# Kernel optimization log

Measured on AMD Instinct MI355X. Metric: run time of the kernel, lower is better.

Reference implementation:

```python
import jax, jax.numpy as jnp
import numpy as np

N_TX, N_USER = 100000, 50000
F_TX, F_USER = 128, 64
HID, H, OUT = 64, 4, 32
E = 500000
SLOPE = 0.2  # PyG GATConv default negative_slope


def _gat(x_src, x_dst, src, dst, W, a_src, a_dst, bias, heads, ch, concat, n_dst):
    # PyG GATConv (shared lin for src/dst, add_self_loops=False)
    hs = (x_src @ W).reshape(-1, heads, ch)          # [Ns,H,C]
    hd = (x_dst @ W).reshape(-1, heads, ch)          # [Nd,H,C]
    als = jnp.einsum('nhc,hc->nh', hs, a_src)        # alpha_src per node
    ald = jnp.einsum('nhc,hc->nh', hd, a_dst)
    e = jax.nn.leaky_relu(als[src] + ald[dst], SLOPE)        # [E,H]
    emax = jax.ops.segment_max(e, dst, num_segments=n_dst)   # softmax per dst
    ex = jnp.exp(e - emax[dst])
    den = jax.ops.segment_sum(ex, dst, num_segments=n_dst)
    alpha = ex / (den[dst] + 1e-16)
    out = jax.ops.segment_sum(hs[src] * alpha[:, :, None], dst, num_segments=n_dst)
    out = out.reshape(n_dst, heads * ch) if concat else out.mean(axis=1)
    return out + bias


def setup_inputs() -> dict:
    key = jax.random.key(0)
    ks = iter(jax.random.split(key, 40))
    def nrm(shape, s=0.05):
        return jax.random.normal(next(ks), shape, dtype=jnp.float32) * s
    inp = {}
    inp['x_tx'] = jax.random.normal(next(ks), (N_TX, F_TX), dtype=jnp.float32)
    inp['x_user'] = jax.random.normal(next(ks), (N_USER, F_USER), dtype=jnp.float32)
    src_u = jax.random.randint(next(ks), (E,), 0, N_USER)
    dst_t = jax.random.randint(next(ks), (E,), 0, N_TX)
    inp['ei_u2t'] = jnp.stack([src_u, dst_t]).astype(jnp.int32)
    src_t = jax.random.randint(next(ks), (E,), 0, N_TX)
    dst_u = jax.random.randint(next(ks), (E,), 0, N_USER)
    inp['ei_t2u'] = jnp.stack([src_t, dst_u]).astype(jnp.int32)
    inp['Wp_tx'] = nrm((F_TX, HID)); inp['bp_tx'] = jnp.zeros((HID,), jnp.float32)
    inp['Wp_user'] = nrm((F_USER, HID)); inp['bp_user'] = jnp.zeros((HID,), jnp.float32)
    for et in ('u2t', 't2u'):
        inp[f'W1_{et}'] = nrm((HID, H * HID))
        inp[f'as1_{et}'] = nrm((H, HID)); inp[f'ad1_{et}'] = nrm((H, HID))
        inp[f'b1_{et}'] = jnp.zeros((H * HID,), jnp.float32)
        inp[f'W2_{et}'] = nrm((H * HID, OUT))
        inp[f'as2_{et}'] = nrm((1, OUT)); inp[f'ad2_{et}'] = nrm((1, OUT))
        inp[f'b2_{et}'] = jnp.zeros((OUT,), jnp.float32)
    inp['Wc'] = nrm((OUT, 1)); inp['bc'] = jnp.zeros((1,), jnp.float32)
    return inp


def reference(x_tx, x_user, ei_u2t, ei_t2u, Wp_tx, bp_tx, Wp_user, bp_user,
              W1_u2t, as1_u2t, ad1_u2t, b1_u2t, W1_t2u, as1_t2u, ad1_t2u, b1_t2u,
              W2_u2t, as2_u2t, ad2_u2t, b2_u2t, W2_t2u, as2_t2u, ad2_t2u, b2_t2u,
              Wc, bc):
    elu = jax.nn.elu
    h_tx = elu(x_tx @ Wp_tx + bp_tx)
    h_us = elu(x_user @ Wp_user + bp_user)
    # conv1: heads=H, concat=True (HeteroConv sum -> each dst has one edge type)
    t1 = _gat(h_us, h_tx, ei_u2t[0], ei_u2t[1], W1_u2t, as1_u2t, ad1_u2t, b1_u2t, H, HID, True, N_TX)
    u1 = _gat(h_tx, h_us, ei_t2u[0], ei_t2u[1], W1_t2u, as1_t2u, ad1_t2u, b1_t2u, H, HID, True, N_USER)
    t1, u1 = elu(t1), elu(u1)
    # conv2: heads=1, concat=False; only 'transaction' output feeds classifier
    t2 = elu(_gat(u1, t1, ei_u2t[0], ei_u2t[1], W2_u2t, as2_u2t, ad2_u2t, b2_u2t, 1, OUT, False, N_TX))
    return (t2 @ Wc + bc)[:, 0]
```

## Files before the change

### kernel.cpp

```cpp
#include <hip/hip_runtime.h>
#include <hip/hip_bf16.h>
#include <math.h>

#define N_TX   100000
#define N_USER 50000
#define F_TX   128
#define F_USER 64
#define HID    64
#define NH     4
#define OUTC   32
#define NE     500000
#define HC1    256
#define SLOPE  0.2f
#define NB_T   391
#define NB_U   196

__device__ __forceinline__ float elu_f(float x) { return x > 0.f ? x : (expf(x) - 1.f); }
__device__ __forceinline__ float lrelu_exp_fast(float x) { x = x > 0.f ? x : SLOPE * x; return __expf(x); }

#define ACC_STEP(i, XS, WV) \
    acc[i][0] = fmaf((XS), (WV).x, acc[i][0]); \
    acc[i][1] = fmaf((XS), (WV).y, acc[i][1]); \
    acc[i][2] = fmaf((XS), (WV).z, acc[i][2]); \
    acc[i][3] = fmaf((XS), (WV).w, acc[i][3]);
#define ACC4(i, XV) \
    ACC_STEP(i, (XV).x, w0) ACC_STEP(i, (XV).y, w1) \
    ACC_STEP(i, (XV).z, w2) ACC_STEP(i, (XV).w, w3)

__global__ __launch_bounds__(256) void gemm_kernel(const float* __restrict__ A,
    const float* __restrict__ B, const float* __restrict__ bias,
    float* __restrict__ C, int N, int K, int M, int act)
{
    __shared__ float As[16][68];
    __shared__ float Bs[16][68];
    const int tid = threadIdx.x;
    const int tx = tid % 16, ty = tid / 16;
    const int row0 = blockIdx.y * 64, col0 = blockIdx.x * 64;
    float acc[4][4] = {};
    for (int k0 = 0; k0 < K; k0 += 16) {
        #pragma unroll
        for (int i = 0; i < 4; ++i) {
            int idx = tid * 4 + i;
            int r = idx >> 4, kk = idx & 15;
            int gr = row0 + r;
            As[kk][r] = (gr < N) ? A[(size_t)gr * K + (k0 + kk)] : 0.f;
        }
        #pragma unroll
        for (int i = 0; i < 4; ++i) {
            int idx = tid * 4 + i;
            int kk = idx >> 6, c = idx & 63;
            int gc = col0 + c;
            Bs[kk][c] = (gc < M) ? B[(size_t)(k0 + kk) * M + gc] : 0.f;
        }
        __syncthreads();
        #pragma unroll 2
        for (int kk = 0; kk < 16; ++kk) {
            const float4 av = *(const float4*)(&As[kk][ty * 4]);
            const float4 bv = *(const float4*)(&Bs[kk][tx * 4]);
            ACC_STEP(0, av.x, bv)
            ACC_STEP(1, av.y, bv)
            ACC_STEP(2, av.z, bv)
            ACC_STEP(3, av.w, bv)
        }
        __syncthreads();
    }
    #pragma unroll
    for (int i = 0; i < 4; ++i) {
        int r = row0 + ty * 4 + i;
        if (r >= N) continue;
        #pragma unroll
        for (int j = 0; j < 4; ++j) {
            int c = col0 + tx * 4 + j;
            if (c >= M) continue;
            float v = acc[i][j] + (bias ? bias[c] : 0.f);
            if (act == 1) v = elu_f(v);
            C[(size_t)r * M + c] = v;
        }
    }
}

__global__ __launch_bounds__(256) void gemm_proj_attn_dual(
    const float* __restrict__ A1, const float* __restrict__ B1, const float* __restrict__ bias1,
    float* __restrict__ C1, int N1, int K1,
    const float* __restrict__ Ma1, float* __restrict__ oa1,
    const float* __restrict__ Mb1, float* __restrict__ ob1, int NB1,
    const float* __restrict__ A2, const float* __restrict__ B2, const float* __restrict__ bias2,
    float* __restrict__ C2, int N2, int K2,
    const float* __restrict__ Ma2, float* __restrict__ oa2,
    const float* __restrict__ Mb2, float* __restrict__ ob2)
{
    __shared__ float As[16][68];
    __shared__ float Bs[16][68];
    const int tid = threadIdx.x;
    const int tx = tid % 16, ty = tid / 16;
    const float* A; const float* B; const float* bias; float* C; int N, K;
    const float* Ma; float* oa; const float* Mb; float* ob; int row0;
    if ((int)blockIdx.y < NB1) {
        A = A1; B = B1; bias = bias1; C = C1; N = N1; K = K1;
        Ma = Ma1; oa = oa1; Mb = Mb1; ob = ob1;
        row0 = blockIdx.y * 64;
    } else {
        A = A2; B = B2; bias = bias2; C = C2; N = N2; K = K2;
        Ma = Ma2; oa = oa2; Mb = Mb2; ob = ob2;
        row0 = (blockIdx.y - NB1) * 64;
    }
    float acc[4][4] = {};
    for (int k0 = 0; k0 < K; k0 += 16) {
        #pragma unroll
        for (int i = 0; i < 4; ++i) {
            int idx = tid * 4 + i;
            int r = idx >> 4, kk = idx & 15;
            int gr = row0 + r;
            As[kk][r] = (gr < N) ? A[(size_t)gr * K + (k0 + kk)] : 0.f;
        }
        #pragma unroll
        for (int i = 0; i < 4; ++i) {
            int idx = tid * 4 + i;
            int kk = idx >> 6, c = idx & 63;
            Bs[kk][c] = B[(size_t)(k0 + kk) * 64 + c];
        }
        __syncthreads();
        #pragma unroll 2
        for (int kk = 0; kk < 16; ++kk) {
            const float4 av = *(const float4*)(&As[kk][ty * 4]);
            const float4 bv = *(const float4*)(&Bs[kk][tx * 4]);
            ACC_STEP(0, av.x, bv)
            ACC_STEP(1, av.y, bv)
            ACC_STEP(2, av.z, bv)
            ACC_STEP(3, av.w, bv)
        }
        __syncthreads();
    }
    const float4 ma0 = *(const float4*)(Ma + (tx * 4 + 0) * 4);
    const float4 ma1 = *(const float4*)(Ma + (tx * 4 + 1) * 4);
    const float4 ma2 = *(const float4*)(Ma + (tx * 4 + 2) * 4);
    const float4 ma3 = *(const float4*)(Ma + (tx * 4 + 3) * 4);
    const float4 mb0 = *(const float4*)(Mb + (tx * 4 + 0) * 4);
    const float4 mb1 = *(const float4*)(Mb + (tx * 4 + 1) * 4);
    const float4 mb2 = *(const float4*)(Mb + (tx * 4 + 2) * 4);
    const float4 mb3 = *(const float4*)(Mb + (tx * 4 + 3) * 4);
    const float4 bb  = *(const float4*)(bias + tx * 4);
    #pragma unroll
    for (int i = 0; i < 4; ++i) {
        int r = row0 + ty * 4 + i;
        bool wr = (r < N);
        float v0 = acc[i][0] + bb.x; v0 = v0 > 0.f ? v0 : (expf(v0) - 1.f);
        float v1 = acc[i][1] + bb.y; v1 = v1 > 0.f ? v1 : (expf(v1) - 1.f);
        float v2 = acc[i][2] + bb.z; v2 = v2 > 0.f ? v2 : (expf(v2) - 1.f);
        float v3 = acc[i][3] + bb.w; v3 = v3 > 0.f ? v3 : (expf(v3) - 1.f);
        if (wr) *(float4*)(C + (size_t)r * 64 + tx * 4) = make_float4(v0, v1, v2, v3);
        float pax = v0 * ma0.x + v1 * ma1.x + v2 * ma2.x + v3 * ma3.x;
        float pay = v0 * ma0.y + v1 * ma1.y + v2 * ma2.y + v3 * ma3.y;
        float paz = v0 * ma0.z + v1 * ma1.z + v2 * ma2.z + v3 * ma3.z;
        float paw = v0 * ma0.w + v1 * ma1.w + v2 * ma2.w + v3 * ma3.w;
        float pbx = v0 * mb0.x + v1 * mb1.x + v2 * mb2.x + v3 * mb3.x;
        float pby = v0 * mb0.y + v1 * mb1.y + v2 * mb2.y + v3 * mb3.y;
        float pbz = v0 * mb0.z + v1 * mb1.z + v2 * mb2.z + v3 * mb3.z;
        float pbw = v0 * mb0.w + v1 * mb1.w + v2 * mb2.w + v3 * mb3.w;
        #pragma unroll
        for (int off = 1; off < 16; off <<= 1) {
            pax += __shfl_xor(pax, off); pay += __shfl_xor(pay, off);
            paz += __shfl_xor(paz, off); paw += __shfl_xor(paw, off);
            pbx += __shfl_xor(pbx, off); pby += __shfl_xor(pby, off);
            pbz += __shfl_xor(pbz, off); pbw += __shfl_xor(pbw, off);
        }
        if (tx == 0 && wr) {
            *(float4*)(oa + (size_t)r * 4) = make_float4(pax, pay, paz, paw);
            *(float4*)(ob + (size_t)r * 4) = make_float4(pbx, pby, pbz, pbw);
        }
    }
}

struct AVArgs  { const float* W; const float* a; float* out; int K; int H; int C; };
struct AVArgs6 { AVArgs t[6]; };

__global__ void attn_vecs_kernel(AVArgs6 args)
{
    AVArgs A = args.t[blockIdx.x];
    int tid = threadIdx.x;
    if (tid < A.K * A.H) {
        int k = tid % A.K, h = tid / A.K;
        float s = 0.f;
        const float* wrow = A.W + (size_t)k * (A.H * A.C) + h * A.C;
        const float* arow = A.a + h * A.C;
        for (int c = 0; c < A.C; ++c) s += wrow[c] * arow[c];
        A.out[k * A.H + h] = s;
    }
}

__global__ __launch_bounds__(256) void hist2_kernel(const int* __restrict__ dst_t,
    const int* __restrict__ dst_u, int* __restrict__ deg_t, int* __restrict__ deg_u)
{
    int e = blockIdx.x * 256 + threadIdx.x;
    if (e < NE) atomicAdd(&deg_t[dst_t[e]], 1);
    else {
        e -= NE;
        if (e < NE) atomicAdd(&deg_u[dst_u[e]], 1);
    }
}

__global__ __launch_bounds__(256) void block_sum2_kernel(const int* __restrict__ deg_t,
    int* __restrict__ bsum_t, const int* __restrict__ deg_u, int* __restrict__ bsum_u)
{
    __shared__ int lds[256];
    int b = blockIdx.x, t = threadIdx.x;
    const int* deg; int* bsum; int Nd, lb;
    if (b < NB_T) { deg = deg_t; bsum = bsum_t; Nd = N_TX; lb = b; }
    else         { deg = deg_u; bsum = bsum_u; Nd = N_USER; lb = b - NB_T; }
    int i = lb * 256 + t;
    lds[t] = (i < Nd) ? deg[i] : 0;
    __syncthreads();
    for (int o = 128; o > 0; o >>= 1) {
        if (t < o) lds[t] += lds[t + o];
        __syncthreads();
    }
    if (t == 0) bsum[lb] = lds[0];
}

__global__ __launch_bounds__(512) void scan_bsum2_kernel(int* __restrict__ bt,
    int* __restrict__ bu)
{
    __shared__ int lds[512];
    int t = threadIdx.x;
    {
        int v = (t < NB_T) ? bt[t] : 0;
        lds[t] = v;
        __syncthreads();
        for (int o = 1; o < 512; o <<= 1) {
            int x = (t >= o) ? lds[t - o] : 0;
            __syncthreads();
            lds[t] += x;
            __syncthreads();
        }
        if (t < NB_T) bt[t] = lds[t] - v;
        __syncthreads();
    }
    {
        int v = (t < NB_U) ? bu[t] : 0;
        lds[t] = v;
        __syncthreads();
        for (int o = 1; o < 512; o <<= 1) {
            int x = (t >= o) ? lds[t - o] : 0;
            __syncthreads();
            lds[t] += x;
            __syncthreads();
        }
        if (t < NB_U) bu[t] = lds[t] - v;
    }
}

__global__ __launch_bounds__(256) void scan_final2_kernel(
    const int* __restrict__ deg_t, const int* __restrict__ be_t,
    int* __restrict__ rowptr_t, int* __restrict__ cur_t,
    const int* __restrict__ deg_u, const int* __restrict__ be_u,
    int* __restrict__ rowptr_u, int* __restrict__ cur_u)
{
    __shared__ int lds[256];
    int b = blockIdx.x, t = threadIdx.x;
    const int* deg; const int* be; int* rowptr; int* cursor; int Nd, lb;
    if (b < NB_T) { deg = deg_t; be = be_t; rowptr = rowptr_t; cursor = cur_t; Nd = N_TX; lb = b; }
    else         { deg = deg_u; be = be_u; rowptr = rowptr_u; cursor = cur_u; Nd = N_USER; lb = b - NB_T; }
    int i = lb * 256 + t;
    int v = (i < Nd) ? deg[i] : 0;
    lds[t] = v;
    __syncthreads();
    for (int o = 1; o < 256; o <<= 1) {
        int x = (t >= o) ? lds[t - o] : 0;
        __syncthreads();
        lds[t] += x;
        __syncthreads();
    }
    int excl = lds[t] - v + be[lb];
    if (i < Nd) {
        rowptr[i] = excl;
        cursor[i] = excl;
        if (i == Nd - 1) rowptr[Nd] = NE;
    }
}

__global__ __launch_bounds__(256) void scatter_ew_kernel(
    const int* __restrict__ src, const int* __restrict__ dst,
    int* __restrict__ cur, float* __restrict__ rec,
    const float* __restrict__ als, const float* __restrict__ ald)
{
    int e = blockIdx.x * 256 + threadIdx.x;
    if (e >= NE) return;
    int s = src[e], d = dst[e];
    int p = atomicAdd(&cur[d], 1);
    float4 a = *(const float4*)(als + (size_t)s * 4);
    float4 b = *(const float4*)(ald + (size_t)d * 4);
    float4 w;
    w.x = lrelu_exp_fast(a.x + b.x);
    w.y = lrelu_exp_fast(a.y + b.y);
    w.z = lrelu_exp_fast(a.z + b.z);
    w.w = lrelu_exp_fast(a.w + b.w);
    float* r8 = rec + (size_t)p * 8;
    *(float4*)(r8)     = w;
    *(float4*)(r8 + 4) = make_float4(__int_as_float(s), 0.f, 0.f, 0.f);
}

__device__ __forceinline__ void acc_edge(int i, int lane,
    const float* __restrict__ rec, const float* __restrict__ hsrc,
    float& a0, float& a1, float& a2, float& a3,
    float& w0, float& w1, float& w2, float& w3)
{
    const float* r8 = rec + (size_t)i * 8;
    float4 e = *(const float4*)(r8);
    int s = __float_as_int(r8[4]);
    float x = hsrc[(size_t)s * 64 + lane];
    a0 = fmaf(e.x, x, a0); w0 += e.x;
    a1 = fmaf(e.y, x, a1); w1 += e.y;
    a2 = fmaf(e.z, x, a2); w2 += e.z;
    a3 = fmaf(e.w, x, a3); w3 += e.w;
}

__global__ __launch_bounds__(256) void agg_conv1_kernel(const int* __restrict__ rowptr,
    const float* __restrict__ rec, const float* __restrict__ hsrc,
    float* __restrict__ agg, int Nd)
{
    int d = blockIdx.x * 4 + (threadIdx.x >> 6);
    int lane = threadIdx.x & 63;
    if (d >= Nd) return;
    int beg = rowptr[d], end = rowptr[d + 1];
    float a0 = 0.f, a1 = 0.f, a2 = 0.f, a3 = 0.f;
    float w0 = 0.f, w1 = 0.f, w2 = 0.f, w3 = 0.f;
    int i = beg;
    for (; i + 2 <= end; i += 2) {
        acc_edge(i,     lane, rec, hsrc, a0, a1, a2, a3, w0, w1, w2, w3);
        acc_edge(i + 1, lane, rec, hsrc, a0, a1, a2, a3, w0, w1, w2, w3);
    }
    if (i < end)
        acc_edge(i, lane, rec, hsrc, a0, a1, a2, a3, w0, w1, w2, w3);
    float* o = agg + (size_t)d * 256;
    o[lane]       = a0 / (w0 + 1e-16f);
    o[64 + lane]  = a1 / (w1 + 1e-16f);
    o[128 + lane] = a2 / (w2 + 1e-16f);
    o[192 + lane] = a3 / (w3 + 1e-16f);
}

__global__ __launch_bounds__(256) void transform_v6(
    const float* __restrict__ agg, const float* __restrict__ W1,
    const float* __restrict__ b1, const float* __restrict__ vvec,
    float* __restrict__ dot_part, float* __restrict__ rows_out,
    int Nd, int writeRows)
{
    constexpr int SXP = 68;
    __shared__ float sX[64 * SXP];
    __shared__ float sW[64 * 64];
    const int tid  = threadIdx.x;
    const int w    = tid >> 6;
    const int lane = tid & 63;
    const int h    = blockIdx.y;
    const int base = blockIdx.x * 64;

    #pragma unroll
    for (int it = 0; it < 4; ++it) {
        int r  = w * 16 + it * 4 + (lane >> 4);
        int c0 = (lane & 15) * 4;
        int g  = base + r;
        float4 v = make_float4(0.f, 0.f, 0.f, 0.f);
        if (g < Nd) v = *(const float4*)(agg + (size_t)g * 256 + h * 64 + c0);
        *(float4*)(sX + r * SXP + c0) = v;
    }
    #pragma unroll
    for (int it = 0; it < 4; ++it) {
        int c    = w * 16 + it * 4 + (lane >> 4);
        int col0 = (lane & 15) * 4;
        *(float4*)(sW + c * 64 + col0) =
            *(const float4*)(W1 + (size_t)c * 256 + h * 64 + col0);
    }
    __syncthreads();

    const int tx = tid & 15;
    const int ty = tid >> 4;
    float acc[4][4] = {};

    #pragma unroll 1
    for (int c0 = 0; c0 < 64; c0 += 4) {
        const float4 x0 = *(const float4*)(sX + (ty * 4 + 0) * SXP + c0);
        const float4 x1 = *(const float4*)(sX + (ty * 4 + 1) * SXP + c0);
        const float4 x2 = *(const float4*)(sX + (ty * 4 + 2) * SXP + c0);
        const float4 x3 = *(const float4*)(sX + (ty * 4 + 3) * SXP + c0);
        const float4 w0 = *(const float4*)(sW + (c0 + 0) * 64 + tx * 4);
        const float4 w1 = *(const float4*)(sW + (c0 + 1) * 64 + tx * 4);
        const float4 w2 = *(const float4*)(sW + (c0 + 2) * 64 + tx * 4);
        const float4 w3 = *(const float4*)(sW + (c0 + 3) * 64 + tx * 4);
        ACC4(0, x0)
        ACC4(1, x1)
        ACC4(2, x2)
        ACC4(3, x3)
    }

    const float4 bb = *(const float4*)(b1   + h * 64 + tx * 4);
    const float4 vv = *(const float4*)(vvec + h * 64 + tx * 4);
    float* dp = dot_part + (size_t)h * Nd;
    #pragma unroll
    for (int i = 0; i < 4; ++i) {
        int g = base + ty * 4 + i;
        if (g >= Nd) continue;
        float v0 = acc[i][0] + bb.x; v0 = v0 > 0.f ? v0 : (expf(v0) - 1.f);
        float v1 = acc[i][1] + bb.y; v1 = v1 > 0.f ? v1 : (expf(v1) - 1.f);
        float v2 = acc[i][2] + bb.z; v2 = v2 > 0.f ? v2 : (expf(v2) - 1.f);
        float v3 = acc[i][3] + bb.w; v3 = v3 > 0.f ? v3 : (expf(v3) - 1.f);
        if (writeRows)
            *(float4*)(rows_out + (size_t)g * 256 + h * 64 + tx * 4) =
                make_float4(v0, v1, v2, v3);
        float s = v0 * vv.x + v1 * vv.y + v2 * vv.z + v3 * vv.w;
        s += __shfl_xor(s, 1); s += __shfl_xor(s, 2);
        s += __shfl_xor(s, 4); s += __shfl_xor(s, 8);
        if (tx == 0) dp[g] = s;
    }
}

__global__ __launch_bounds__(256) void combine_parts(
    const float* __restrict__ ap, float* __restrict__ o1, int N1,
    const float* __restrict__ bp, float* __restrict__ o2, int N2)
{
    int i = blockIdx.x * 256 + threadIdx.x;
    if (i < N1) {
        o1[i] = ap[i] + ap[N1 + i] + ap[2 * N1 + i] + ap[3 * N1 + i];
    } else {
        int j = i - N1;
        if (j < N2)
            o2[j] = bp[j] + bp[N2 + j] + bp[2 * N2 + j] + bp[3 * N2 + j];
    }
}

__global__ __launch_bounds__(256) void conv2_fused_kernel(const int* __restrict__ rowptr,
    const float* __restrict__ rec, const float* __restrict__ hs2,
    const float* __restrict__ als2, const float* __restrict__ ald2,
    const float* __restrict__ b2, const float* __restrict__ Wc, const float* __restrict__ bc,
    float* __restrict__ out, int Nd)
{
    int d = blockIdx.x * 4 + (threadIdx.x >> 6);
    int lane = threadIdx.x & 63;
    if (d >= Nd) return;
    int beg = rowptr[d], end = rowptr[d + 1];
    float aldd = ald2[d];
    int half = lane >> 5, c = lane & 31;
    float acc = 0.f, wsum = 0.f;
    for (int i = beg + half; i < end; i += 2) {
        int s = __float_as_int(rec[(size_t)i * 8 + 4]);
        float w = lrelu_exp_fast(als2[s] + aldd);
        acc = fmaf(w, hs2[(size_t)s * 32 + c], acc);
        wsum += w;
    }
    acc  += __shfl_down(acc, 32);
    wsum += __shfl_down(wsum, 32);
    float val = 0.f;
    if (lane < 32) {
        float t2 = acc / (wsum + 1e-16f) + b2[c];
        t2 = t2 > 0.f ? t2 : (expf(t2) - 1.f);
        val = t2 * Wc[c];
    }
    #pragma unroll
    for (int o = 16; o > 0; o >>= 1) val += __shfl_down(val, o);
    if (lane == 0) out[d] = val + bc[0];
}

extern "C" void kernel_launch(void* const* d_in, const int* in_sizes, int n_in,
                              void* d_out, int out_size, void* d_ws, size_t ws_size,
                              hipStream_t stream)
{
    const float* x_tx    = (const float*)d_in[0];
    const float* x_user  = (const float*)d_in[1];
    const int*   ei_u2t  = (const int*)d_in[2];
    const int*   ei_t2u  = (const int*)d_in[3];
    const float* Wp_tx   = (const float*)d_in[4];
    const float* bp_tx   = (const float*)d_in[5];
    const float* Wp_user = (const float*)d_in[6];
    const float* bp_user = (const float*)d_in[7];
    const float* W1_u2t  = (const float*)d_in[8];
    const float* as1_u2t = (const float*)d_in[9];
    const float* ad1_u2t = (const float*)d_in[10];
    const float* b1_u2t  = (const float*)d_in[11];
    const float* W2_u2t  = (const float*)d_in[12];
    const float* as2_u2t = (const float*)d_in[13];
    const float* ad2_u2t = (const float*)d_in[14];
    const float* b2_u2t  = (const float*)d_in[15];
    const float* W1_t2u  = (const float*)d_in[16];
    const float* as1_t2u = (const float*)d_in[17];
    const float* ad1_t2u = (const float*)d_in[18];
    const float* b1_t2u  = (const float*)d_in[19];
    const float* Wc      = (const float*)d_in[24];
    const float* bc      = (const float*)d_in[25];
    float* out = (float*)d_out;
    float* ws  = (float*)d_ws;

    const int* src_u2t = ei_u2t;
    const int* dst_u2t = ei_u2t + NE;
    const int* src_t2u = ei_t2u;
    const int* dst_u   = ei_t2u + NE;

    float* h_tx   = ws;
    float* h_us   = ws + 6400000;
    float* hs2    = ws + 9600000;
    float* als2   = ws + 11200000;
    float* ald2   = ws + 11250000;
    float* als_us = ws + 11350000;
    float* ald_us = ws + 11550000;
    float* als_tx = ws + 11750000;
    float* ald_tx = ws + 12150000;
    float* agg    = ws + 12550000;
    float* avec   = ws + 38150000;
    float* ald2p = hs2;
    float* als2p = hs2 + 400000;
    float* rec_t  = ws + 38152000;
    float* rec_u  = agg + 12800000;
    int* ibase    = (int*)(ws + 42152000);
    int* deg_t    = ibase;
    int* deg_u    = ibase + 100000;
    int* rowptr_t = ibase + 150000;
    int* cur_t    = ibase + 250001;
    int* rowptr_u = ibase + 350001;
    int* cur_u    = ibase + 400002;
    int* bsum_t   = ibase + 450052;
    int* bsum_u   = ibase + 450564;

    float* Msrc_u2t = avec + 0;
    float* Mdst_u2t = avec + 256;
    float* Msrc_t2u = avec + 512;
    float* Mdst_t2u = avec + 768;
    float* vsrc2    = avec + 1024;
    float* vdst2    = avec + 1280;

    AVArgs6 av;
    av.t[0] = { W1_u2t, as1_u2t, Msrc_u2t, HID, NH, HID };
    av.t[1] = { W1_u2t, ad1_u2t, Mdst_u2t, HID, NH, HID };
    av.t[2] = { W1_t2u, as1_t2u, Msrc_t2u, HID, NH, HID };
    av.t[3] = { W1_t2u, ad1_t2u, Mdst_t2u, HID, NH, HID };
    av.t[4] = { W2_u2t, as2_u2t, vsrc2, HC1, 1, OUTC };
    av.t[5] = { W2_u2t, ad2_u2t, vdst2, HC1, 1, OUTC };
    attn_vecs_kernel<<<6, 256, 0, stream>>>(av);

    hipMemsetAsync(deg_t, 0, 150000 * sizeof(int), stream);

    hist2_kernel<<<(2 * NE + 255) / 256, 256, 0, stream>>>(dst_u2t, dst_u, deg_t, deg_u);
    block_sum2_kernel<<<NB_T + NB_U, 256, 0, stream>>>(deg_t, bsum_t, deg_u, bsum_u);
    scan_bsum2_kernel<<<1, 512, 0, stream>>>(bsum_t, bsum_u);
    scan_final2_kernel<<<NB_T + NB_U, 256, 0, stream>>>(
        deg_t, bsum_t, rowptr_t, cur_t, deg_u, bsum_u, rowptr_u, cur_u);

    const int NB1 = (N_TX + 63) / 64;
    const int NB2 = (N_USER + 63) / 64;
    gemm_proj_attn_dual<<<dim3(1, NB1 + NB2), 256, 0, stream>>>(
        x_tx, Wp_tx, bp_tx, h_tx, N_TX, F_TX,
        Mdst_u2t, ald_tx, Msrc_t2u, als_tx, NB1,
        x_user, Wp_user, bp_user, h_us, N_USER, F_USER,
        Msrc_u2t, als_us, Mdst_t2u, ald_us);

    scatter_ew_kernel<<<(NE + 255) / 256, 256, 0, stream>>>(
        src_u2t, dst_u2t, cur_t, rec_t, als_us, ald_tx);
    agg_conv1_kernel<<<(N_TX + 3) / 4, 256, 0, stream>>>(
        rowptr_t, rec_t, h_us, agg, N_TX);
    transform_v6<<<dim3((N_TX + 63) / 64, NH), 256, 0, stream>>>(
        agg, W1_u2t, b1_u2t, vdst2, ald2p, nullptr, N_TX, 0);

    scatter_ew_kernel<<<(NE + 255) / 256, 256, 0, stream>>>(
        src_t2u, dst_u, cur_u, rec_u, als_tx, ald_us);
    agg_conv1_kernel<<<(N_USER + 3) / 4, 256, 0, stream>>>(
        rowptr_u, rec_u, h_tx, agg, N_USER);
    transform_v6<<<dim3((N_USER + 63) / 64, NH), 256, 0, stream>>>(
        agg, W1_t2u, b1_t2u, vsrc2, als2p, agg, N_USER, 1);
    float* u1 = agg;

    combine_parts<<<(N_TX + N_USER + 255) / 256, 256, 0, stream>>>(
        ald2p, ald2, N_TX, als2p, als2, N_USER);

    gemm_kernel<<<dim3(1, (N_USER + 63) / 64), 256, 0, stream>>>(
        u1, W2_u2t, nullptr, hs2, N_USER, HC1, OUTC, 0);
    conv2_fused_kernel<<<(N_TX + 3) / 4, 256, 0, stream>>>(
        rowptr_t, rec_t, hs2, als2, ald2, b2_u2t, Wc, bc, out, N_TX);
}
```

Baseline: 564.2 us.

## Fuse conv2 linear projection into per-head conv1 transform with partial sums

The user-side conv1 transform no longer writes the full 256-wide u1 rows to global memory. Each head block instead keeps its ELU output in shared memory and multiplies it by its 64-row slice of W2, writing per-head partial hs2 values. A combined reduction kernel then sums the four partials, alongside the existing attention-dot partial sums. This removes the u1 write and re-read and the separate GEMM launch, at the cost of writing and re-reading four 32-wide partial buffers.

```diff
diff --git a/kernel.cpp b/kernel.cpp
--- a/kernel.cpp
+++ b/kernel.cpp
@@ -26,58 +26,6 @@
 #define ACC4(i, XV) \
     ACC_STEP(i, (XV).x, w0) ACC_STEP(i, (XV).y, w1) \
     ACC_STEP(i, (XV).z, w2) ACC_STEP(i, (XV).w, w3)
-
-__global__ __launch_bounds__(256) void gemm_kernel(const float* __restrict__ A,
-    const float* __restrict__ B, const float* __restrict__ bias,
-    float* __restrict__ C, int N, int K, int M, int act)
-{
-    __shared__ float As[16][68];
-    __shared__ float Bs[16][68];
-    const int tid = threadIdx.x;
-    const int tx = tid % 16, ty = tid / 16;
-    const int row0 = blockIdx.y * 64, col0 = blockIdx.x * 64;
-    float acc[4][4] = {};
-    for (int k0 = 0; k0 < K; k0 += 16) {
-        #pragma unroll
-        for (int i = 0; i < 4; ++i) {
-            int idx = tid * 4 + i;
-            int r = idx >> 4, kk = idx & 15;
-            int gr = row0 + r;
-            As[kk][r] = (gr < N) ? A[(size_t)gr * K + (k0 + kk)] : 0.f;
-        }
-        #pragma unroll
-        for (int i = 0; i < 4; ++i) {
-            int idx = tid * 4 + i;
-            int kk = idx >> 6, c = idx & 63;
-            int gc = col0 + c;
-            Bs[kk][c] = (gc < M) ? B[(size_t)(k0 + kk) * M + gc] : 0.f;
-        }
-        __syncthreads();
-        #pragma unroll 2
-        for (int kk = 0; kk < 16; ++kk) {
-            const float4 av = *(const float4*)(&As[kk][ty * 4]);
-            const float4 bv = *(const float4*)(&Bs[kk][tx * 4]);
-            ACC_STEP(0, av.x, bv)
-            ACC_STEP(1, av.y, bv)
-            ACC_STEP(2, av.z, bv)
-            ACC_STEP(3, av.w, bv)
-        }
-        __syncthreads();
-    }
-    #pragma unroll
-    for (int i = 0; i < 4; ++i) {
-        int r = row0 + ty * 4 + i;
-        if (r >= N) continue;
-        #pragma unroll
-        for (int j = 0; j < 4; ++j) {
-            int c = col0 + tx * 4 + j;
-            if (c >= M) continue;
-            float v = acc[i][j] + (bias ? bias[c] : 0.f);
-            if (act == 1) v = elu_f(v);
-            C[(size_t)r * M + c] = v;
-        }
-    }
-}
 
 __global__ __launch_bounds__(256) void gemm_proj_attn_dual(
     const float* __restrict__ A1, const float* __restrict__ B1, const float* __restrict__ bias1,
@@ -338,11 +286,11 @@
     o[192 + lane] = a3 / (w3 + 1e-16f);
 }
 
-__global__ __launch_bounds__(256) void transform_v6(
+__global__ __launch_bounds__(256) void transform_v10(
     const float* __restrict__ agg, const float* __restrict__ W1,
     const float* __restrict__ b1, const float* __restrict__ vvec,
-    float* __restrict__ dot_part, float* __restrict__ rows_out,
-    int Nd, int writeRows)
+    float* __restrict__ dot_part, const float* __restrict__ W2,
+    float* __restrict__ hs2p, int Nd, int fuse2)
 {
     constexpr int SXP = 68;
     __shared__ float sX[64 * SXP];
@@ -390,6 +338,7 @@
         ACC4(2, x2)
         ACC4(3, x3)
     }
+    __syncthreads();
 
     const float4 bb = *(const float4*)(b1   + h * 64 + tx * 4);
     const float4 vv = *(const float4*)(vvec + h * 64 + tx * 4);
@@ -397,32 +346,73 @@
     #pragma unroll
     for (int i = 0; i < 4; ++i) {
         int g = base + ty * 4 + i;
-        if (g >= Nd) continue;
         float v0 = acc[i][0] + bb.x; v0 = v0 > 0.f ? v0 : (expf(v0) - 1.f);
         float v1 = acc[i][1] + bb.y; v1 = v1 > 0.f ? v1 : (expf(v1) - 1.f);
         float v2 = acc[i][2] + bb.z; v2 = v2 > 0.f ? v2 : (expf(v2) - 1.f);
         float v3 = acc[i][3] + bb.w; v3 = v3 > 0.f ? v3 : (expf(v3) - 1.f);
-        if (writeRows)
-            *(float4*)(rows_out + (size_t)g * 256 + h * 64 + tx * 4) =
-                make_float4(v0, v1, v2, v3);
+        if (fuse2)
+            *(float4*)(sX + (ty * 4 + i) * SXP + tx * 4) = make_float4(v0, v1, v2, v3);
         float s = v0 * vv.x + v1 * vv.y + v2 * vv.z + v3 * vv.w;
         s += __shfl_xor(s, 1); s += __shfl_xor(s, 2);
         s += __shfl_xor(s, 4); s += __shfl_xor(s, 8);
-        if (tx == 0) dp[g] = s;
-    }
-}
-
-__global__ __launch_bounds__(256) void combine_parts(
-    const float* __restrict__ ap, float* __restrict__ o1, int N1,
-    const float* __restrict__ bp, float* __restrict__ o2, int N2)
+        if (tx == 0 && g < Nd) dp[g] = s;
+    }
+
+    if (!fuse2) return;
+
+    {
+        int idx0 = tid * 8;
+        int r = idx0 >> 5, j0 = idx0 & 31;
+        const float* wsrc = W2 + (size_t)(h * 64 + r) * 32 + j0;
+        *(float4*)(sW + r * 32 + j0)     = *(const float4*)(wsrc);
+        *(float4*)(sW + r * 32 + j0 + 4) = *(const float4*)(wsrc + 4);
+    }
+    __syncthreads();
+
+    float a2[4][2] = {};
+    #pragma unroll 1
+    for (int r0 = 0; r0 < 64; r0 += 4) {
+        const float4 y0 = *(const float4*)(sX + (ty * 4 + 0) * SXP + r0);
+        const float4 y1 = *(const float4*)(sX + (ty * 4 + 1) * SXP + r0);
+        const float4 y2 = *(const float4*)(sX + (ty * 4 + 2) * SXP + r0);
+        const float4 y3 = *(const float4*)(sX + (ty * 4 + 3) * SXP + r0);
+        const float2 wA = *(const float2*)(sW + (r0 + 0) * 32 + tx * 2);
+        const float2 wB = *(const float2*)(sW + (r0 + 1) * 32 + tx * 2);
+        const float2 wC = *(const float2*)(sW + (r0 + 2) * 32 + tx * 2);
+        const float2 wD = *(const float2*)(sW + (r0 + 3) * 32 + tx * 2);
+        #define P2(i, YV) \
+            a2[i][0] = fmaf((YV).x, wA.x, a2[i][0]); a2[i][1] = fmaf((YV).x, wA.y, a2[i][1]); \
+            a2[i][0] = fmaf((YV).y, wB.x, a2[i][0]); a2[i][1] = fmaf((YV).y, wB.y, a2[i][1]); \
+            a2[i][0] = fmaf((YV).z, wC.x, a2[i][0]); a2[i][1] = fmaf((YV).z, wC.y, a2[i][1]); \
+            a2[i][0] = fmaf((YV).w, wD.x, a2[i][0]); a2[i][1] = fmaf((YV).w, wD.y, a2[i][1]);
+        P2(0, y0) P2(1, y1) P2(2, y2) P2(3, y3)
+        #undef P2
+    }
+    float* hp = hs2p + (size_t)h * ((size_t)N_USER * 32);
+    #pragma unroll
+    for (int i = 0; i < 4; ++i) {
+        int g = base + ty * 4 + i;
+        if (g < Nd)
+            *(float2*)(hp + (size_t)g * 32 + tx * 2) = make_float2(a2[i][0], a2[i][1]);
+    }
+}
+
+__global__ __launch_bounds__(256) void combine3_kernel(
+    const float* __restrict__ ap, float* __restrict__ o1,
+    const float* __restrict__ bp, float* __restrict__ o2,
+    const float* __restrict__ hp, float* __restrict__ o3)
 {
     int i = blockIdx.x * 256 + threadIdx.x;
-    if (i < N1) {
-        o1[i] = ap[i] + ap[N1 + i] + ap[2 * N1 + i] + ap[3 * N1 + i];
+    if (i < N_TX) {
+        o1[i] = ap[i] + ap[N_TX + i] + ap[2 * N_TX + i] + ap[3 * N_TX + i];
+    } else if (i < N_TX + N_USER) {
+        int j = i - N_TX;
+        o2[j] = bp[j] + bp[N_USER + j] + bp[2 * N_USER + j] + bp[3 * N_USER + j];
     } else {
-        int j = i - N1;
-        if (j < N2)
-            o2[j] = bp[j] + bp[N2 + j] + bp[2 * N2 + j] + bp[3 * N2 + j];
+        int k = i - N_TX - N_USER;
+        const int HS = N_USER * 32;
+        if (k < HS)
+            o3[k] = hp[k] + hp[HS + k] + hp[2 * HS + k] + hp[3 * HS + k];
     }
 }
 
@@ -494,7 +484,7 @@
 
     float* h_tx   = ws;
     float* h_us   = ws + 6400000;
-    float* hs2    = ws + 9600000;
+    float* parts  = ws + 9600000;
     float* als2   = ws + 11200000;
     float* ald2   = ws + 11250000;
     float* als_us = ws + 11350000;
@@ -503,10 +493,12 @@
     float* ald_tx = ws + 12150000;
     float* agg    = ws + 12550000;
     float* avec   = ws + 38150000;
-    float* ald2p = hs2;
-    float* als2p = hs2 + 400000;
+    float* ald2p = parts;
+    float* als2p = parts + 400000;
     float* rec_t  = ws + 38152000;
     float* rec_u  = agg + 12800000;
+    float* hs2p   = agg + 17000000;
+    float* hs2f   = agg + 23500000;
     int* ibase    = (int*)(ws + 42152000);
     int* deg_t    = ibase;
     int* deg_u    = ibase + 100000;
@@ -553,22 +545,19 @@
         src_u2t, dst_u2t, cur_t, rec_t, als_us, ald_tx);
     agg_conv1_kernel<<<(N_TX + 3) / 4, 256, 0, stream>>>(
         rowptr_t, rec_t, h_us, agg, N_TX);
-    transform_v6<<<dim3((N_TX + 63) / 64, NH), 256, 0, stream>>>(
-        agg, W1_u2t, b1_u2t, vdst2, ald2p, nullptr, N_TX, 0);
+    transform_v10<<<dim3((N_TX + 63) / 64, NH), 256, 0, stream>>>(
+        agg, W1_u2t, b1_u2t, vdst2, ald2p, nullptr, nullptr, N_TX, 0);
 
     scatter_ew_kernel<<<(NE + 255) / 256, 256, 0, stream>>>(
         src_t2u, dst_u, cur_u, rec_u, als_tx, ald_us);
     agg_conv1_kernel<<<(N_USER + 3) / 4, 256, 0, stream>>>(
         rowptr_u, rec_u, h_tx, agg, N_USER);
-    transform_v6<<<dim3((N_USER + 63) / 64, NH), 256, 0, stream>>>(
-        agg, W1_t2u, b1_t2u, vsrc2, als2p, agg, N_USER, 1);
-    float* u1 = agg;
-
-    combine_parts<<<(N_TX + N_USER + 255) / 256, 256, 0, stream>>>(
-        ald2p, ald2, N_TX, als2p, als2, N_USER);
-
-    gemm_kernel<<<dim3(1, (N_USER + 63) / 64), 256, 0, stream>>>(
-        u1, W2_u2t, nullptr, hs2, N_USER, HC1, OUTC, 0);
+    transform_v10<<<dim3((N_USER + 63) / 64, NH), 256, 0, stream>>>(
+        agg, W1_t2u, b1_t2u, vsrc2, als2p, W2_u2t, hs2p, N_USER, 1);
+
+    combine3_kernel<<<(N_TX + N_USER + N_USER * 32 + 255) / 256, 256, 0, stream>>>(
+        ald2p, ald2, als2p, als2, hs2p, hs2f);
+
     conv2_fused_kernel<<<(N_TX + 3) / 4, 256, 0, stream>>>(
-        rowptr_t, rec_t, hs2, als2, ald2, b2_u2t, Wc, bc, out, N_TX);
-}
+        rowptr_t, rec_t, hs2f, als2, ald2, b2_u2t, Wc, bc, out, N_TX);
+}
```

Measured after the change: 538.5 us. 4.6% less time.
